# Optimization experiments

Measured on AMD Instinct MI355X. Metric: run time of the kernel, lower is better.

The kernel has to match this reference:

```python
import jax, jax.numpy as jnp
import numpy as np

B, T, F, U = 32768, 7, 36, 256

def setup_inputs() -> dict:
    key = jax.random.key(0)
    ks = jax.random.split(key, 5)
    x = jax.random.normal(ks[0], (B, T, F), dtype=jnp.float32)
    h0 = jax.random.normal(ks[1], (B, U), dtype=jnp.float32)
    c0 = jax.random.normal(ks[2], (B, U), dtype=jnp.float32)
    Wk = jax.random.normal(ks[3], (F, 4 * U), dtype=jnp.float32) * 0.1
    Wr = jax.random.normal(ks[4], (U, 4 * U), dtype=jnp.float32) * 0.05
    b = jnp.zeros((4 * U,), dtype=jnp.float32)
    return {"x": x, "h0": h0, "c0": c0, "Wk": Wk, "Wr": Wr, "b": b}

def reference(x, h0, c0, Wk, Wr, b):
    # Precompute input projection for all 7 steps: [B,T,4U]
    zx = jnp.einsum('btf,fg->btg', x, Wk) + b
    zx_t = jnp.transpose(zx, (1, 0, 2))  # time-major [T,B,4U]

    def step(carry, z_in):
        h, c = carry
        z = z_in + h @ Wr  # [B,4U]
        i, f, g, o = jnp.split(z, 4, axis=-1)  # Keras gate order i,f,g,o
        i = jax.nn.sigmoid(i)
        f = jax.nn.sigmoid(f)
        g = jnp.tanh(g)
        o = jax.nn.sigmoid(o)
        c_new = f * c + i * g
        h_new = o * jnp.tanh(c_new)
        return (h_new, c_new), h_new

    (_, _), hs = jax.lax.scan(step, (h0, c0), zx_t)
    return jnp.transpose(hs, (1, 0, 2))  # [B,T,U] (return_sequences=True)
```

## Files before the change

kernel.cpp:

```cpp
#include <hip/hip_runtime.h>

typedef _Float16 half8 __attribute__((ext_vector_type(8)));
typedef float f32x4 __attribute__((ext_vector_type(4)));

#define B_TOTAL 32768
#define T 7
#define F 36
#define U 256
#define G4 1024
#define BM 64
#define KC 10
#define KPACK 32
#define H_STRIDE 264
#define XS 72

__global__ __launch_bounds__(1024) void pack_w(const float* __restrict__ Wr,
                                               const float* __restrict__ Wk,
                                               _Float16* __restrict__ Wq) {
    const int kc   = blockIdx.x >> 2;
    const int kin0 = (blockIdx.x & 3) * 8;
    const int n    = threadIdx.x;
    _Float16* dst = Wq + ((size_t)kc * G4 + n) * KPACK + kin0;
    #pragma unroll
    for (int j = 0; j < 8; ++j) {
        int k = kc * KPACK + kin0 + j;
        float v = 0.f;
        if (k < U)          v = Wr[(size_t)k * G4 + n];
        else if (k < U + F) v = Wk[(size_t)(k - U) * G4 + n];
        dst[j] = (_Float16)v;
    }
}

__device__ __forceinline__ float fast_sigmoid(float x) {
    return __builtin_amdgcn_rcpf(1.f + __expf(-x));
}
__device__ __forceinline__ float fast_tanh(float x) {
    return 1.f - 2.f * __builtin_amdgcn_rcpf(1.f + __expf(2.f * x));
}

__global__ __launch_bounds__(1024) void lstm_kernel(
    const float* __restrict__ x,
    const float* __restrict__ h0,
    const float* __restrict__ c0,
    const _Float16* __restrict__ Wq,
    const float* __restrict__ bias_g,
    float* __restrict__ out)
{
    __shared__ __align__(16) _Float16 hbuf[2][BM * H_STRIDE];
    __shared__ __align__(16) _Float16 xs[T * BM * XS];

    const int tid  = threadIdx.x;
    const int lane = tid & 63;
    const int w    = tid >> 6;
    const int l15  = lane & 15;
    const int q    = lane >> 4;
    const int u0   = w * 16;
    const int b0   = blockIdx.x * BM;

    {
        half8 z = {};
        for (int i = tid * 8; i < T * BM * XS; i += 1024 * 8)
            *(half8*)&xs[i] = z;
    }
    __syncthreads();

    for (int i = tid; i < BM * U; i += 1024) {
        int m = i >> 8, u = i & 255;
        hbuf[0][m * H_STRIDE + u] = (_Float16)h0[(size_t)b0 * U + i];
    }
    for (int i = tid; i < BM * (T * F); i += 1024) {
        int row = i / (T * F);
        int rem = i - row * (T * F);
        int t   = rem / F;
        int f   = rem - t * F;
        xs[(t * BM + row) * XS + f] = (_Float16)x[(size_t)(b0 + row) * (T * F) + rem];
    }
    float c[16];
    #pragma unroll
    for (int mt = 0; mt < 4; ++mt)
        #pragma unroll
        for (int r = 0; r < 4; ++r) {
            int row = mt * 16 + q * 4 + r;
            c[mt * 4 + r] = c0[(size_t)(b0 + row) * U + u0 + l15];
        }
    float bv[4];
    #pragma unroll
    for (int g = 0; g < 4; ++g) bv[g] = bias_g[g * U + u0 + l15];

    __syncthreads();

    int cur = 0;
    #pragma unroll 1
    for (int t = 0; t < T; ++t) {
        f32x4 acc[4][4];
        #pragma unroll
        for (int mt = 0; mt < 4; ++mt)
            #pragma unroll
            for (int g = 0; g < 4; ++g)
                acc[mt][g] = (f32x4){bv[g], bv[g], bv[g], bv[g]};

        #pragma unroll 2
        for (int kc = 0; kc < KC; ++kc) {
            half8 bf[4];
            #pragma unroll
            for (int g = 0; g < 4; ++g) {
                size_t off = ((size_t)kc * G4 + g * U + u0 + l15) * KPACK + q * 8;
                bf[g] = *(const half8*)(Wq + off);
            }
            #pragma unroll
            for (int mt = 0; mt < 4; ++mt) {
                half8 af;
                if (kc < 8)
                    af = *(const half8*)&hbuf[cur][(mt * 16 + l15) * H_STRIDE + kc * 32 + q * 8];
                else
                    af = *(const half8*)&xs[(t * BM + mt * 16 + l15) * XS + (kc - 8) * 32 + q * 8];
                #pragma unroll
                for (int g = 0; g < 4; ++g)
                    acc[mt][g] = __builtin_amdgcn_mfma_f32_16x16x32_f16(af, bf[g], acc[mt][g], 0, 0, 0);
            }
        }

        const int nxt = cur ^ 1;
        #pragma unroll
        for (int mt = 0; mt < 4; ++mt)
            #pragma unroll
            for (int r = 0; r < 4; ++r) {
                float zi = acc[mt][0][r];
                float zf = acc[mt][1][r];
                float zg = acc[mt][2][r];
                float zo = acc[mt][3][r];
                float ig = fast_sigmoid(zi);
                float fg = fast_sigmoid(zf);
                float gg = fast_tanh(zg);
                float og = fast_sigmoid(zo);
                float cn = fg * c[mt * 4 + r] + ig * gg;
                c[mt * 4 + r] = cn;
                float hv = og * fast_tanh(cn);
                int row = mt * 16 + q * 4 + r;
                hbuf[nxt][row * H_STRIDE + u0 + l15] = (_Float16)hv;
            }

        __syncthreads();

        #pragma unroll
        for (int rb = 0; rb < 2; ++rb) {
            int j   = tid + rb * 1024;
            int row = j >> 5;
            int uo  = (j & 31) * 8;
            half8 hv = *(const half8*)&hbuf[nxt][row * H_STRIDE + uo];
            f32x4 lo = { (float)hv[0], (float)hv[1], (float)hv[2], (float)hv[3] };
            f32x4 hi = { (float)hv[4], (float)hv[5], (float)hv[6], (float)hv[7] };
            float* dst = out + ((size_t)(b0 + row) * T + t) * U + uo;
            __builtin_nontemporal_store(lo, (f32x4*)dst);
            __builtin_nontemporal_store(hi, (f32x4*)(dst + 4));
        }

        cur = nxt;
    }
}

extern "C" void kernel_launch(void* const* d_in, const int* in_sizes, int n_in,
                              void* d_out, int out_size, void* d_ws, size_t ws_size,
                              hipStream_t stream) {
    const float* x  = (const float*)d_in[0];
    const float* h0 = (const float*)d_in[1];
    const float* c0 = (const float*)d_in[2];
    const float* Wk = (const float*)d_in[3];
    const float* Wr = (const float*)d_in[4];
    const float* b  = (const float*)d_in[5];
    float* out = (float*)d_out;

    _Float16* Wq = (_Float16*)d_ws;

    pack_w<<<KC * 4, 1024, 0, stream>>>(Wr, Wk, Wq);
    lstm_kernel<<<B_TOTAL / BM, 1024, 0, stream>>>(x, h0, c0, Wq, b, out);
}
```

Measured before the change: 489.4 us.

## Split batch tile into two halves and overlap matmul with gate math

Halves the block to 512 threads, with each wave covering 32 units instead of 16. The 64-row batch tile is split into two 32-row halves whose recurrent matmuls and gate computations are interleaved, so one half's MFMA work can overlap the other half's transcendental gate math and stores. Each B-fragment of the weights is now reused across two M tiles instead of four, and there are twice as many syncthreads per step. Launch bounds ask for 2 blocks per CU, which constrains registers, and the doubled accumulator sets risk spilling.

```diff
diff --git a/kernel.cpp b/kernel.cpp
--- a/kernel.cpp
+++ b/kernel.cpp
@@ -9,6 +9,7 @@
 #define U 256
 #define G4 1024
 #define BM 64
+#define THREADS 512
 #define KC 10
 #define KPACK 32
 #define H_STRIDE 264
@@ -38,7 +39,7 @@
     return 1.f - 2.f * __builtin_amdgcn_rcpf(1.f + __expf(2.f * x));
 }
 
-__global__ __launch_bounds__(1024) void lstm_kernel(
+__global__ __launch_bounds__(512, 2) void lstm_kernel(
     const float* __restrict__ x,
     const float* __restrict__ h0,
     const float* __restrict__ c0,
@@ -46,7 +47,8 @@
     const float* __restrict__ bias_g,
     float* __restrict__ out)
 {
-    __shared__ __align__(16) _Float16 hbuf[2][BM * H_STRIDE];
+    __shared__ __align__(16) _Float16 hA[2][32 * H_STRIDE];
+    __shared__ __align__(16) _Float16 hB[2][32 * H_STRIDE];
     __shared__ __align__(16) _Float16 xs[T * BM * XS];
 
     const int tid  = threadIdx.x;
@@ -54,108 +56,144 @@
     const int w    = tid >> 6;
     const int l15  = lane & 15;
     const int q    = lane >> 4;
-    const int u0   = w * 16;
+    const int u0   = w * 32;
     const int b0   = blockIdx.x * BM;
 
     {
         half8 z = {};
-        for (int i = tid * 8; i < T * BM * XS; i += 1024 * 8)
+        for (int i = tid * 8; i < T * BM * XS; i += THREADS * 8)
             *(half8*)&xs[i] = z;
     }
     __syncthreads();
 
-    for (int i = tid; i < BM * U; i += 1024) {
+    for (int i = tid; i < BM * U; i += THREADS) {
         int m = i >> 8, u = i & 255;
-        hbuf[0][m * H_STRIDE + u] = (_Float16)h0[(size_t)b0 * U + i];
-    }
-    for (int i = tid; i < BM * (T * F); i += 1024) {
+        _Float16 v = (_Float16)h0[(size_t)b0 * U + i];
+        if (m < 32) hA[0][m * H_STRIDE + u] = v;
+        else        hB[0][(m - 32) * H_STRIDE + u] = v;
+    }
+    for (int i = tid; i < BM * (T * F); i += THREADS) {
         int row = i / (T * F);
         int rem = i - row * (T * F);
         int t   = rem / F;
         int f   = rem - t * F;
         xs[(t * BM + row) * XS + f] = (_Float16)x[(size_t)(b0 + row) * (T * F) + rem];
     }
-    float c[16];
+    float cA[16], cB[16];
     #pragma unroll
-    for (int mt = 0; mt < 4; ++mt)
-        #pragma unroll
-        for (int r = 0; r < 4; ++r) {
-            int row = mt * 16 + q * 4 + r;
-            c[mt * 4 + r] = c0[(size_t)(b0 + row) * U + u0 + l15];
-        }
-    float bv[4];
+    for (int mt = 0; mt < 2; ++mt)
+        #pragma unroll
+        for (int nt = 0; nt < 2; ++nt)
+            #pragma unroll
+            for (int r = 0; r < 4; ++r) {
+                int idx = mt * 8 + nt * 4 + r;
+                int row = mt * 16 + q * 4 + r;
+                int u   = u0 + nt * 16 + l15;
+                cA[idx] = c0[(size_t)(b0 + row) * U + u];
+                cB[idx] = c0[(size_t)(b0 + 32 + row) * U + u];
+            }
+    float bv[4][2];
     #pragma unroll
-    for (int g = 0; g < 4; ++g) bv[g] = bias_g[g * U + u0 + l15];
+    for (int g = 0; g < 4; ++g)
+        #pragma unroll
+        for (int nt = 0; nt < 2; ++nt)
+            bv[g][nt] = bias_g[g * 256 + u0 + nt * 16 + l15];
 
     __syncthreads();
 
-    int cur = 0;
-    #pragma unroll 1
-    for (int t = 0; t < T; ++t) {
-        f32x4 acc[4][4];
-        #pragma unroll
-        for (int mt = 0; mt < 4; ++mt)
-            #pragma unroll
-            for (int g = 0; g < 4; ++g)
-                acc[mt][g] = (f32x4){bv[g], bv[g], bv[g], bv[g]};
-
+    f32x4 pA[2][8], pB[2][8];
+
+    auto kstep = [&](f32x4 (&P)[2][8], const _Float16* hbase, int xrow0) {
+        #pragma unroll
+        for (int mt = 0; mt < 2; ++mt)
+            #pragma unroll
+            for (int gnt = 0; gnt < 8; ++gnt) {
+                float v = bv[gnt >> 1][gnt & 1];
+                P[mt][gnt] = (f32x4){v, v, v, v};
+            }
         #pragma unroll 2
         for (int kc = 0; kc < KC; ++kc) {
-            half8 bf[4];
-            #pragma unroll
-            for (int g = 0; g < 4; ++g) {
-                size_t off = ((size_t)kc * G4 + g * U + u0 + l15) * KPACK + q * 8;
-                bf[g] = *(const half8*)(Wq + off);
-            }
-            #pragma unroll
-            for (int mt = 0; mt < 4; ++mt) {
-                half8 af;
+            half8 af[2];
+            #pragma unroll
+            for (int mt = 0; mt < 2; ++mt) {
                 if (kc < 8)
-                    af = *(const half8*)&hbuf[cur][(mt * 16 + l15) * H_STRIDE + kc * 32 + q * 8];
+                    af[mt] = *(const half8*)&hbase[(mt * 16 + l15) * H_STRIDE + kc * 32 + q * 8];
                 else
-                    af = *(const half8*)&xs[(t * BM + mt * 16 + l15) * XS + (kc - 8) * 32 + q * 8];
+                    af[mt] = *(const half8*)&xs[(size_t)(xrow0 + mt * 16 + l15) * XS + (kc - 8) * 32 + q * 8];
+            }
+            #pragma unroll
+            for (int bb = 0; bb < 2; ++bb) {
+                half8 bf[4];
                 #pragma unroll
-                for (int g = 0; g < 4; ++g)
-                    acc[mt][g] = __builtin_amdgcn_mfma_f32_16x16x32_f16(af, bf[g], acc[mt][g], 0, 0, 0);
+                for (int j = 0; j < 4; ++j) {
+                    int gnt = bb * 4 + j;
+                    size_t off = ((size_t)kc * G4 + (gnt >> 1) * 256 + u0 + (gnt & 1) * 16 + l15) * KPACK + q * 8;
+                    bf[j] = *(const half8*)(Wq + off);
+                }
+                #pragma unroll
+                for (int mt = 0; mt < 2; ++mt)
+                    #pragma unroll
+                    for (int j = 0; j < 4; ++j)
+                        P[mt][bb * 4 + j] = __builtin_amdgcn_mfma_f32_16x16x32_f16(af[mt], bf[j], P[mt][bb * 4 + j], 0, 0, 0);
             }
         }
-
-        const int nxt = cur ^ 1;
-        #pragma unroll
-        for (int mt = 0; mt < 4; ++mt)
-            #pragma unroll
-            for (int r = 0; r < 4; ++r) {
-                float zi = acc[mt][0][r];
-                float zf = acc[mt][1][r];
-                float zg = acc[mt][2][r];
-                float zo = acc[mt][3][r];
-                float ig = fast_sigmoid(zi);
-                float fg = fast_sigmoid(zf);
-                float gg = fast_tanh(zg);
-                float og = fast_sigmoid(zo);
-                float cn = fg * c[mt * 4 + r] + ig * gg;
-                c[mt * 4 + r] = cn;
-                float hv = og * fast_tanh(cn);
-                int row = mt * 16 + q * 4 + r;
-                hbuf[nxt][row * H_STRIDE + u0 + l15] = (_Float16)hv;
-            }
-
-        __syncthreads();
-
+    };
+
+    auto gates = [&](f32x4 (&P)[2][8], float (&cc)[16], _Float16* hnxt) {
+        #pragma unroll
+        for (int mt = 0; mt < 2; ++mt)
+            #pragma unroll
+            for (int nt = 0; nt < 2; ++nt)
+                #pragma unroll
+                for (int r = 0; r < 4; ++r) {
+                    int idx = mt * 8 + nt * 4 + r;
+                    float zi = P[mt][0 + nt][r];
+                    float zf = P[mt][2 + nt][r];
+                    float zg = P[mt][4 + nt][r];
+                    float zo = P[mt][6 + nt][r];
+                    float ig = fast_sigmoid(zi);
+                    float fg = fast_sigmoid(zf);
+                    float gg = fast_tanh(zg);
+                    float og = fast_sigmoid(zo);
+                    float cn = fg * cc[idx] + ig * gg;
+                    cc[idx] = cn;
+                    float hv = og * fast_tanh(cn);
+                    hnxt[(mt * 16 + q * 4 + r) * H_STRIDE + u0 + nt * 16 + l15] = (_Float16)hv;
+                }
+    };
+
+    auto outst = [&](const _Float16* hsrc, int halfbase, int t) {
         #pragma unroll
         for (int rb = 0; rb < 2; ++rb) {
-            int j   = tid + rb * 1024;
+            int j   = tid + rb * THREADS;
             int row = j >> 5;
             int uo  = (j & 31) * 8;
-            half8 hv = *(const half8*)&hbuf[nxt][row * H_STRIDE + uo];
+            half8 hv = *(const half8*)&hsrc[row * H_STRIDE + uo];
             f32x4 lo = { (float)hv[0], (float)hv[1], (float)hv[2], (float)hv[3] };
             f32x4 hi = { (float)hv[4], (float)hv[5], (float)hv[6], (float)hv[7] };
-            float* dst = out + ((size_t)(b0 + row) * T + t) * U + uo;
+            float* dst = out + ((size_t)(b0 + halfbase + row) * T + t) * U + uo;
             __builtin_nontemporal_store(lo, (f32x4*)dst);
             __builtin_nontemporal_store(hi, (f32x4*)(dst + 4));
         }
-
-        cur = nxt;
+    };
+
+    int curA = 0, curB = 0;
+
+    kstep(pA, hA[0], 0);
+
+    #pragma unroll 1
+    for (int t = 0; t < T; ++t) {
+        kstep(pB, hB[curB], t * BM + 32);
+        gates(pA, cA, hA[curA ^ 1]);
+        __syncthreads();
+        outst(hA[curA ^ 1], 0, t);
+        curA ^= 1;
+
+        if (t + 1 < T) kstep(pA, hA[curA], (t + 1) * BM);
+        gates(pB, cB, hB[curB ^ 1]);
+        __syncthreads();
+        outst(hB[curB ^ 1], 32, t);
+        curB ^= 1;
     }
 }
 
@@ -173,5 +211,5 @@
     _Float16* Wq = (_Float16*)d_ws;
 
     pack_w<<<KC * 4, 1024, 0, stream>>>(Wr, Wk, Wq);
-    lstm_kernel<<<B_TOTAL / BM, 1024, 0, stream>>>(x, h0, c0, Wq, b, out);
-}
+    lstm_kernel<<<B_TOTAL / BM, THREADS, 0, stream>>>(x, h0, c0, Wq, b, out);
+}
```

New measurement: 651.5 us. +33.1%, slower.
